# Optimization experiments

Measured on AMD Instinct MI355X. Metric: run time of the kernel, lower is better.

## Reference

```python
import jax, jax.numpy as jnp
import numpy as np
from functools import partial

LEAK = 1.0 / 3.0   # scn default leakiness 0.333
EPS = 1e-4         # scn BatchNormalization default eps


def linkey(c, S):
    return (c[..., 0] * S + c[..., 1]) * S + c[..., 2]


def sub_offsets(K):
    r = K // 2
    g = np.stack(np.meshgrid(*([np.arange(-r, r + 1)] * 3), indexing='ij'), -1).reshape(-1, 3)
    return jnp.asarray(g, jnp.int32)


def down_offsets(s):
    g = np.stack(np.meshgrid(*([np.arange(s)] * 3), indexing='ij'), -1).reshape(-1, 3)
    return jnp.asarray(g, jnp.int32)


@partial(jax.checkpoint, static_argnums=(4, 5))
def sparse_conv(out_coords, in_coords, in_feats, W, S_in, stride, offsets):
    """Rulebook gather-GEMM-scatter via sorted-key binary search.
    out_coords [M,3], in_coords [N,3] sorted by linearized key, in_feats [N,Cin],
    W [K3,Cin,Cout]. Submanifold: stride=1, centered offsets, out_coords==in_coords.
    Strided scn.Convolution: offsets 0..stride-1, out sites = unique(in//stride)."""
    in_keys = linkey(in_coords, S_in)  # sorted [N]
    Nin = in_keys.shape[0]

    def body(acc, kw):
        off, Wk = kw
        child = out_coords * stride + off                       # [M,3]
        valid = jnp.all((child >= 0) & (child < S_in), axis=-1)
        nkey = linkey(child, S_in)
        idx = jnp.searchsorted(in_keys, nkey)
        idxc = jnp.clip(idx, 0, Nin - 1)
        found = valid & (in_keys[idxc] == nkey)
        g = jnp.where(found[:, None], in_feats[idxc], 0.0)      # gather, zero for inactive
        return acc + g @ Wk, None

    acc0 = jnp.zeros((out_coords.shape[0], W.shape[-1]), in_feats.dtype)
    acc, _ = jax.lax.scan(body, acc0, (offsets, W))
    return acc


def bn_lrelu(x, g, b):
    m = x.mean(0)
    v = x.var(0)
    y = (x - m) * (g / jnp.sqrt(v + EPS)) + b
    return jnp.where(y > 0, y, LEAK * y)


def lrelu(x):
    return jnp.where(x > 0, x, LEAK * x)


def forward_core(floats, c0, c1, c2, c3, c4):
    (feats0, W_init, Wd1, gd1, bd1, W11a, g11, b11, W11b,
     W12a, g12, b12, W12b, Wd2, gd2, bd2,
     W21a, g21, b21, W21b, W22a, g22, b22, W22b,
     Wd3, gd3, bd3, Wd4, gd4, bd4, W2, b2, W3, b3) = floats
    o3 = sub_offsets(3)
    x = sparse_conv(c0, c0, feats0, W_init, 512, 1, sub_offsets(7))                 # [N0,64] @512
    x = bn_lrelu(sparse_conv(c1, c0, x, Wd1, 512, 2, down_offsets(2)), gd1, bd1)    # [N1,64] @256
    res = x
    h = bn_lrelu(sparse_conv(c1, c1, x, W11a, 256, 1, o3), g11, b11)
    x = lrelu(sparse_conv(c1, c1, h, W11b, 256, 1, o3) + res)
    res = x
    h = bn_lrelu(sparse_conv(c1, c1, x, W12a, 256, 1, o3), g12, b12)
    x = lrelu(sparse_conv(c1, c1, h, W12b, 256, 1, o3) + res)
    x = bn_lrelu(sparse_conv(c2, c1, x, Wd2, 256, 2, down_offsets(2)), gd2, bd2)    # [N2,128] @128
    res = x
    h = bn_lrelu(sparse_conv(c2, c2, x, W21a, 128, 1, o3), g21, b21)
    x = lrelu(sparse_conv(c2, c2, h, W21b, 128, 1, o3) + res)
    res = x
    h = bn_lrelu(sparse_conv(c2, c2, x, W22a, 128, 1, o3), g22, b22)
    x = lrelu(sparse_conv(c2, c2, h, W22b, 128, 1, o3) + res)
    x = bn_lrelu(sparse_conv(c3, c2, x, Wd3, 128, 4, down_offsets(4)), gd3, bd3)    # [N3,64] @32
    x = bn_lrelu(sparse_conv(c4, c3, x, Wd4, 32, 4, down_offsets(4)), gd4, bd4)     # [N4,2]  @8
    # SparseToDense -> dense [2,8,8,8], then torch .view(-1, 2*8*8*8) (channel-major)
    k4 = linkey(c4, 8)
    dense = jnp.zeros((8 * 8 * 8, 2), x.dtype).at[k4].set(x)    # [512,2]
    flat = dense.T.reshape(1, -1)                               # [1,1024]
    v = jax.nn.elu(flat @ W2 + b2)
    return jax.nn.sigmoid(v @ W3 + b3)                          # [1,1]


def _decode(k, S):
    a = k // (S * S)
    r = k % (S * S)
    return np.stack([a, r // S, r % S], -1).astype(np.int32)


def setup_inputs() -> dict:
    rng = np.random.default_rng(0)
    N0 = 50000
    k0 = np.unique(rng.integers(0, 512 ** 3, size=N0 + 20000))[:N0]
    c0 = _decode(k0, 512)
    c1 = _decode(np.unique((c0[:, 0].astype(np.int64) // 2 * 256 + c0[:, 1] // 2) * 256 + c0[:, 2] // 2), 256)
    c2 = _decode(np.unique((c1[:, 0].astype(np.int64) // 2 * 128 + c1[:, 1] // 2) * 128 + c1[:, 2] // 2), 128)
    c3 = _decode(np.unique((c2[:, 0].astype(np.int64) // 4 * 32 + c2[:, 1] // 4) * 32 + c2[:, 2] // 4), 32)
    c4 = _decode(np.unique((c3[:, 0].astype(np.int64) // 4 * 8 + c3[:, 1] // 4) * 8 + c3[:, 2] // 4), 8)
    key = jax.random.key(0)
    ks = jax.random.split(key, 20)

    def w(i, shape, fan):
        return jax.random.normal(ks[i], shape, jnp.float32) / np.float32(np.sqrt(fan))

    return dict(
        feats0=jax.random.normal(ks[0], (N0, 1), jnp.float32),
        W_init=w(1, (343, 1, 64), 343.0),
        Wd1=w(2, (8, 64, 64), 8 * 64), gd1=jnp.ones(64), bd1=jnp.zeros(64),
        W11a=w(3, (27, 64, 64), 27 * 64), g11=jnp.ones(64), b11=jnp.zeros(64),
        W11b=w(4, (27, 64, 64), 27 * 64),
        W12a=w(5, (27, 64, 64), 27 * 64), g12=jnp.ones(64), b12=jnp.zeros(64),
        W12b=w(6, (27, 64, 64), 27 * 64),
        Wd2=w(7, (8, 64, 128), 8 * 64), gd2=jnp.ones(128), bd2=jnp.zeros(128),
        W21a=w(8, (27, 128, 128), 27 * 128), g21=jnp.ones(128), b21=jnp.zeros(128),
        W21b=w(9, (27, 128, 128), 27 * 128),
        W22a=w(10, (27, 128, 128), 27 * 128), g22=jnp.ones(128), b22=jnp.zeros(128),
        W22b=w(11, (27, 128, 128), 27 * 128),
        Wd3=w(12, (64, 128, 64), 64 * 128), gd3=jnp.ones(64), bd3=jnp.zeros(64),
        Wd4=w(13, (64, 64, 2), 64 * 64), gd4=jnp.ones(2), bd4=jnp.zeros(2),
        W2=w(14, (1024, 2), 1024.0), b2=jnp.zeros(2),
        W3=w(15, (2, 1), 2.0), b3=jnp.zeros(1),
        coords0=jnp.asarray(c0), coords1=jnp.asarray(c1), coords2=jnp.asarray(c2),
        coords3=jnp.asarray(c3), coords4=jnp.asarray(c4),
    )


def reference(feats0, W_init, Wd1, gd1, bd1, W11a, g11, b11, W11b, W12a, g12, b12, W12b,
              Wd2, gd2, bd2, W21a, g21, b21, W21b, W22a, g22, b22, W22b,
              Wd3, gd3, bd3, Wd4, gd4, bd4, W2, b2, W3, b3,
              coords0, coords1, coords2, coords3, coords4):
    floats = (feats0, W_init, Wd1, gd1, bd1, W11a, g11, b11, W11b, W12a, g12, b12, W12b,
              Wd2, gd2, bd2, W21a, g21, b21, W21b, W22a, g22, b22, W22b,
              Wd3, gd3, bd3, Wd4, gd4, bd4, W2, b2, W3, b3)
    return forward_core(floats, coords0, coords1, coords2, coords3, coords4)
```

## Files before the change

### kernel.cpp

```cpp
#include <hip/hip_runtime.h>

#define LEAKF (1.0f/3.0f)
#define BN_EPS 1e-4f

__device__ __forceinline__ unsigned hmix(int key) {
    unsigned h = (unsigned)key * 2654435761u;
    h ^= h >> 15;
    return h;
}

__device__ __forceinline__ int hlookup(const int* __restrict__ hk,
                                       const int* __restrict__ hv,
                                       int mask, int key) {
    unsigned h = hmix(key) & (unsigned)mask;
    while (true) {
        int k = hk[h];
        if (k == key) return hv[h];
        if (k == -1) return -1;
        h = (h + 1) & (unsigned)mask;
    }
}

__device__ __forceinline__ float bnl(float v, float s, float h) {
    v = v * s + h;
    return v > 0.f ? v : v * LEAKF;
}

__global__ __launch_bounds__(256) void build_hash_bm_all(
    int B0, int B1, int B2,
    int N0, const int* __restrict__ c0, int* __restrict__ hk0, int* __restrict__ hv0,
    int m0, unsigned* __restrict__ bm0,
    int N1, const int* __restrict__ c1, int* __restrict__ hk1, int* __restrict__ hv1,
    int m1, unsigned* __restrict__ bm1,
    int N2, const int* __restrict__ c2, int* __restrict__ hk2, int* __restrict__ hv2,
    int m2, unsigned* __restrict__ bm2,
    int N3, const int* __restrict__ c3, int* __restrict__ hk3, int* __restrict__ hv3,
    int m3) {
    const int* coords; int* hk; int* hv; unsigned* bm; int mask, S, N, i;
    int b = blockIdx.x;
    if (b < B0)           { coords = c0; hk = hk0; hv = hv0; bm = bm0; mask = m0; S = 512; N = N0; i = b * 256 + threadIdx.x; }
    else if (b < B0 + B1) { coords = c1; hk = hk1; hv = hv1; bm = bm1; mask = m1; S = 256; N = N1; i = (b - B0) * 256 + threadIdx.x; }
    else if (b < B0 + B1 + B2) { coords = c2; hk = hk2; hv = hv2; bm = bm2; mask = m2; S = 128; N = N2; i = (b - B0 - B1) * 256 + threadIdx.x; }
    else                  { coords = c3; hk = hk3; hv = hv3; bm = nullptr; mask = m3; S = 32; N = N3; i = (b - B0 - B1 - B2) * 256 + threadIdx.x; }
    if (i >= N) return;
    int key = (coords[3 * i] * S + coords[3 * i + 1]) * S + coords[3 * i + 2];
    if (bm) atomicOr(&bm[key >> 5], 1u << (key & 31));
    unsigned h = hmix(key) & (unsigned)mask;
    while (true) {
        int old = atomicCAS(&hk[h], -1, key);
        if (old == -1 || old == key) { hv[h] = i; break; }
        h = (h + 1) & (unsigned)mask;
    }
}

__global__ __launch_bounds__(256) void rb_sub_bm(
    int B1,
    int N1, const int* __restrict__ c1, const unsigned* __restrict__ bm1,
    const int* __restrict__ hk1, const int* __restrict__ hv1, int m1,
    int2* __restrict__ rb1, int* __restrict__ cnt1, int cap1,
    int N2, const int* __restrict__ c2, const unsigned* __restrict__ bm2,
    const int* __restrict__ hk2, const int* __restrict__ hv2, int m2,
    int2* __restrict__ rb2, int* __restrict__ cnt2, int cap2) {
    __shared__ int lcnt[27];
    __shared__ int lbase[27];
    int tid = threadIdx.x;
    if (tid < 27) lcnt[tid] = 0;
    __syncthreads();
    const int* coords; const unsigned* bm; const int* hk; const int* hv;
    int mask, S, N, t; int2* pairs; int* counts; int cap;
    if (blockIdx.x < B1) {
        coords = c1; bm = bm1; hk = hk1; hv = hv1; mask = m1; S = 256; N = N1;
        pairs = rb1; counts = cnt1; cap = cap1; t = blockIdx.x * 256 + tid;
    } else {
        coords = c2; bm = bm2; hk = hk2; hv = hv2; mask = m2; S = 128; N = N2;
        pairs = rb2; counts = cnt2; cap = cap2; t = (blockIdx.x - B1) * 256 + tid;
    }
    unsigned bits = 0;
    int m = 0, kmin = 0, z = 0, dx = 0, dy = 0;
    int rk[3], ix[3];
    if (t < N * 9) {
        m = t / 9;
        int od = t - m * 9;
        dx = od / 3 - 1;
        dy = od - (od / 3) * 3 - 1;
        int x = coords[3 * m] + dx;
        int y = coords[3 * m + 1] + dy;
        z = coords[3 * m + 2];
        if ((unsigned)x < (unsigned)S && (unsigned)y < (unsigned)S) {
            int zmin = z - 1 < 0 ? 0 : z - 1;
            int zmax = z + 1 > S - 1 ? S - 1 : z + 1;
            kmin = (x * S + y) * S + zmin;
            int wi = kmin >> 5, sh = kmin & 31, nb = zmax - zmin + 1;
            unsigned long long w =
                ((unsigned long long)bm[wi + 1] << 32) | (unsigned long long)bm[wi];
            bits = (unsigned)((w >> sh) & ((1u << nb) - 1u));
            if (dx == 0 && dy == 0) bits &= ~(1u << (z - zmin));
            unsigned tmp = bits;
            int nf = 0;
            while (tmp) {
                int bb = __ffs(tmp) - 1;
                tmp &= tmp - 1;
                ix[nf] = hlookup(hk, hv, mask, kmin + bb);
                int dz = (kmin & (S - 1)) + bb - z;
                int k = (dx + 1) * 9 + (dy + 1) * 3 + (dz + 1);
                rk[nf] = atomicAdd(&lcnt[k], 1);
                nf++;
            }
        }
    }
    __syncthreads();
    if (tid < 27 && lcnt[tid] > 0) lbase[tid] = atomicAdd(&counts[tid], lcnt[tid]);
    __syncthreads();
    {
        unsigned tmp = bits;
        int j = 0;
        while (tmp) {
            int bb = __ffs(tmp) - 1;
            tmp &= tmp - 1;
            int dz = (kmin & (S - 1)) + bb - z;
            int k = (dx + 1) * 9 + (dy + 1) * 3 + (dz + 1);
            int p = lbase[k] + rk[j];
            if (p < cap) pairs[(size_t)k * cap + p] = make_int2(m, ix[j]);
            j++;
        }
    }
}

__global__ __launch_bounds__(256) void rb_down_all(
    int B1, int B2,
    int N0, const int* __restrict__ c0, const int* __restrict__ hk1,
    const int* __restrict__ hv1, int m1, int2* __restrict__ rbD1,
    int* __restrict__ cntD1, int capD1,
    int N1, const int* __restrict__ c1, const int* __restrict__ hk2,
    const int* __restrict__ hv2, int m2, int2* __restrict__ rbD2,
    int* __restrict__ cntD2, int capD2,
    int N2, const int* __restrict__ c2, const int* __restrict__ hk3,
    const int* __restrict__ hv3, int m3, int2* __restrict__ rbD3,
    int* __restrict__ cntD3, int capD3) {
    __shared__ int lcnt[64];
    __shared__ int lbase[64];
    int tid = threadIdx.x;
    const int* cin; const int* hk; const int* hv;
    int mask, Sout, s, Nin, i; int2* pairs; int* counts; int cap;
    int b = blockIdx.x;
    if (b < B1) {
        cin = c0; hk = hk1; hv = hv1; mask = m1; Sout = 256; s = 2; Nin = N0;
        pairs = rbD1; counts = cntD1; cap = capD1; i = b * 256 + tid;
    } else if (b < B1 + B2) {
        cin = c1; hk = hk2; hv = hv2; mask = m2; Sout = 128; s = 2; Nin = N1;
        pairs = rbD2; counts = cntD2; cap = capD2; i = (b - B1) * 256 + tid;
    } else {
        cin = c2; hk = hk3; hv = hv3; mask = m3; Sout = 32; s = 4; Nin = N2;
        pairs = rbD3; counts = cntD3; cap = capD3; i = (b - B1 - B2) * 256 + tid;
    }
    int K3 = s * s * s;
    if (tid < K3) lcnt[tid] = 0;
    __syncthreads();
    int k = -1, m = -1, rank = 0;
    if (i < Nin) {
        int x = cin[3 * i], y = cin[3 * i + 1], z = cin[3 * i + 2];
        k = ((x % s) * s + (y % s)) * s + (z % s);
        int key = ((x / s) * Sout + (y / s)) * Sout + (z / s);
        m = hlookup(hk, hv, mask, key);
        rank = atomicAdd(&lcnt[k], 1);
    }
    __syncthreads();
    if (tid < K3 && lcnt[tid] > 0) lbase[tid] = atomicAdd(&counts[tid], lcnt[tid]);
    __syncthreads();
    if (i < Nin) {
        int p = lbase[k] + rank;
        if (p < cap) pairs[(size_t)k * cap + p] = make_int2(m, i);
    }
}

__global__ __launch_bounds__(256) void init_probe(
    int total, int chunk, const int* __restrict__ c0, const unsigned* __restrict__ bm,
    const int* __restrict__ hk, const int* __restrict__ hv, int mask,
    int2* __restrict__ pairs, int* __restrict__ pcount, int cap) {
    __shared__ int lcnt, lbase;
    int tid = threadIdx.x;
    if (tid == 0) lcnt = 0;
    __syncthreads();
    int b = blockIdx.x;
    int nb = (b & 7) * chunk + (b >> 3);
    int t = nb * 256 + tid;
    unsigned bits = 0;
    int m = -1, kmin = 0, z = 0, dx = 0, dy = 0, rank = 0;
    if (t < total) {
        m = t / 49;
        int od = t - m * 49;
        dx = od / 7 - 3;
        dy = od - (od / 7) * 7 - 3;
        int x = c0[3 * m] + dx;
        int y = c0[3 * m + 1] + dy;
        z = c0[3 * m + 2];
        if ((unsigned)x < 512u && (unsigned)y < 512u) {
            int zmin = z - 3 < 0 ? 0 : z - 3;
            int zmax = z + 3 > 511 ? 511 : z + 3;
            kmin = (x * 512 + y) * 512 + zmin;
            int wi = kmin >> 5, sh = kmin & 31, nb2 = zmax - zmin + 1;
            unsigned long long w =
                ((unsigned long long)bm[wi + 1] << 32) | (unsigned long long)bm[wi];
            bits = (unsigned)((w >> sh) & ((1u << nb2) - 1u));
            if (dx == 0 && dy == 0) bits &= ~(1u << (z - zmin));
            if (bits) rank = atomicAdd(&lcnt, __popc(bits));
        }
    }
    __syncthreads();
    if (tid == 0 && lcnt > 0) lbase = atomicAdd(pcount, lcnt);
    __syncthreads();
    while (bits) {
        int b2 = __ffs(bits) - 1;
        bits &= bits - 1;
        int nkey = kmin + b2;
        int idx = hlookup(hk, hv, mask, nkey);
        int dz = (kmin & 511) + b2 - z;
        int k = (dx + 3) * 49 + (dy + 3) * 7 + (dz + 3);
        int p = lbase + rank++;
        if (p < cap) pairs[p] = make_int2(m, idx | (k << 17));
    }
}

__global__ __launch_bounds__(256) void init_center(
    int N0, const float* __restrict__ f0, const float* __restrict__ W,
    float* __restrict__ out) {
    int t = blockIdx.x * 256 + threadIdx.x;
    if (t >= N0 * 64) return;
    int m = t >> 6, co = t & 63;
    out[t] = f0[m] * W[171 * 64 + co];
}

__global__ __launch_bounds__(256) void init_apply(
    const int2* __restrict__ pairs, const int* __restrict__ pcount, int cap,
    const float* __restrict__ f0, const float* __restrict__ W,
    float* __restrict__ out) {
    int P = min(*pcount, cap);
    int t = blockIdx.x * 256 + threadIdx.x;
    if (t >= P * 64) return;
    int p = t >> 6, co = t & 63;
    int2 pr = pairs[p];
    int idx = pr.y & 0x1FFFF, k = pr.y >> 17;
    atomicAdd(&out[(size_t)pr.x * 64 + co], f0[idx] * W[k * 64 + co]);
}

template <int C, int TS, bool BNF>
__global__ __launch_bounds__(256) void center_gemm(
    int N, const float* __restrict__ inF, const float* __restrict__ Wc,
    float* __restrict__ out, const float* __restrict__ scp,
    const float* __restrict__ shp) {
    constexpr int C4 = C / 4;
    constexpr int SP = TS / 8;
    __shared__ float sW[C * 64];
    __shared__ float4 sRow[TS * C4];
    int tid = threadIdx.x;
    int t0 = blockIdx.x * TS;
    int co0 = blockIdx.y << 6;
    for (int e = tid; e < C * 16; e += 256) {
        int ci = e >> 4, c4 = e & 15;
        ((float4*)sW)[e] = *(const float4*)(Wc + (size_t)ci * C + co0 + c4 * 4);
    }
    for (int e = tid; e < TS * C4; e += 256) {
        int p = e / C4, c4 = e - p * C4;
        float4 v = make_float4(0.f, 0.f, 0.f, 0.f);
        if (t0 + p < N) {
            v = ((const float4*)inF)[(size_t)(t0 + p) * C4 + c4];
            if (BNF) {
                float4 s4 = ((const float4*)scp)[c4];
                float4 h4 = ((const float4*)shp)[c4];
                v.x = bnl(v.x, s4.x, h4.x);
                v.y = bnl(v.y, s4.y, h4.y);
                v.z = bnl(v.z, s4.z, h4.z);
                v.w = bnl(v.w, s4.w, h4.w);
            }
        }
        sRow[e] = v;
    }
    __syncthreads();
    int co = tid & 31, sg = tid >> 5;
    float accA[SP], accB[SP];
#pragma unroll
    for (int j = 0; j < SP; j++) { accA[j] = 0.f; accB[j] = 0.f; }
    for (int c4 = 0; c4 < C4; c4++) {
        float a0 = sW[(c4 * 4 + 0) * 64 + co];
        float a1 = sW[(c4 * 4 + 1) * 64 + co];
        float a2 = sW[(c4 * 4 + 2) * 64 + co];
        float a3 = sW[(c4 * 4 + 3) * 64 + co];
        float b0 = sW[(c4 * 4 + 0) * 64 + co + 32];
        float b1 = sW[(c4 * 4 + 1) * 64 + co + 32];
        float b2 = sW[(c4 * 4 + 2) * 64 + co + 32];
        float b3 = sW[(c4 * 4 + 3) * 64 + co + 32];
#pragma unroll
        for (int j = 0; j < SP; j++) {
            float4 r = sRow[(sg * SP + j) * C4 + c4];
            accA[j] += r.x * a0 + r.y * a1 + r.z * a2 + r.w * a3;
            accB[j] += r.x * b0 + r.y * b1 + r.z * b2 + r.w * b3;
        }
    }
#pragma unroll
    for (int j = 0; j < SP; j++) {
        int p = sg * SP + j;
        if (t0 + p < N) {
            out[(size_t)(t0 + p) * C + co0 + co] = accA[j];
            out[(size_t)(t0 + p) * C + co0 + co + 32] = accB[j];
        }
    }
}

template <int CIN, int P, int MODE>
__global__ __launch_bounds__(256) void pair_gemm(
    const float* __restrict__ inF, const float* __restrict__ inF2,
    const float* __restrict__ W, float* __restrict__ out,
    const int2* __restrict__ pairs, const int* __restrict__ counts,
    int cap, int chunksPerK, int totalNb, int COUT,
    const float* __restrict__ scp, const float* __restrict__ shp) {
    constexpr int C4 = CIN / 4;
    constexpr int SP = P / 8;
    __shared__ float sW[CIN * 64];
    __shared__ float4 sRow[P * C4];
    __shared__ int sM[P];
    __shared__ int sIdx[P];
    int b = blockIdx.x;
    int nb = (b & 7) * (gridDim.x >> 3) + (b >> 3);
    if (nb >= totalNb) return;
    int k = nb / chunksPerK;
    int chunk = nb - k * chunksPerK;
    int cnt = min(counts[k], cap);
    int base = chunk * P;
    if (base >= cnt) return;
    int Pact = min(P, cnt - base);
    int tid = threadIdx.x;
    if (tid < P) {
        if (tid < Pact) {
            int2 pr = pairs[(size_t)k * cap + base + tid];
            sM[tid] = pr.x;
            sIdx[tid] = pr.y;
        } else {
            sM[tid] = -1;
            sIdx[tid] = 0;
        }
    }
    __syncthreads();
    int co0 = blockIdx.y << 6;
    const float* gW = W + (size_t)k * CIN * COUT + co0;
    for (int e = tid; e < CIN * 16; e += 256) {
        int ci = e >> 4, c4 = e & 15;
        ((float4*)sW)[e] = *(const float4*)(gW + (size_t)ci * COUT + c4 * 4);
    }
    for (int e = tid; e < P * C4; e += 256) {
        int p = e / C4, c4 = e - p * C4;
        float4 v = make_float4(0.f, 0.f, 0.f, 0.f);
        if (p < Pact) {
            v = ((const float4*)inF)[(size_t)sIdx[p] * C4 + c4];
            if (MODE == 1) {
                float4 s4 = ((const float4*)scp)[c4];
                float4 h4 = ((const float4*)shp)[c4];
                v.x = bnl(v.x, s4.x, h4.x);
                v.y = bnl(v.y, s4.y, h4.y);
                v.z = bnl(v.z, s4.z, h4.z);
                v.w = bnl(v.w, s4.w, h4.w);
            } else if (MODE == 2) {
                float4 u = ((const float4*)inF2)[(size_t)sIdx[p] * C4 + c4];
                v.x += u.x; v.y += u.y; v.z += u.z; v.w += u.w;
                v.x = v.x > 0.f ? v.x : v.x * LEAKF;
                v.y = v.y > 0.f ? v.y : v.y * LEAKF;
                v.z = v.z > 0.f ? v.z : v.z * LEAKF;
                v.w = v.w > 0.f ? v.w : v.w * LEAKF;
            }
        }
        sRow[e] = v;
    }
    __syncthreads();
    int co = tid & 31, sg = tid >> 5;
    float accA[SP], accB[SP];
#pragma unroll
    for (int j = 0; j < SP; j++) { accA[j] = 0.f; accB[j] = 0.f; }
    for (int c4 = 0; c4 < C4; c4++) {
        float a0 = sW[(c4 * 4 + 0) * 64 + co];
        float a1 = sW[(c4 * 4 + 1) * 64 + co];
        float a2 = sW[(c4 * 4 + 2) * 64 + co];
        float a3 = sW[(c4 * 4 + 3) * 64 + co];
        float b0 = sW[(c4 * 4 + 0) * 64 + co + 32];
        float b1 = sW[(c4 * 4 + 1) * 64 + co + 32];
        float b2 = sW[(c4 * 4 + 2) * 64 + co + 32];
        float b3 = sW[(c4 * 4 + 3) * 64 + co + 32];
#pragma unroll
        for (int j = 0; j < SP; j++) {
            float4 r = sRow[(sg * SP + j) * C4 + c4];
            accA[j] += r.x * a0 + r.y * a1 + r.z * a2 + r.w * a3;
            accB[j] += r.x * b0 + r.y * b1 + r.z * b2 + r.w * b3;
        }
    }
#pragma unroll
    for (int j = 0; j < SP; j++) {
        int p = sg * SP + j;
        if (p < Pact) {
            atomicAdd(&out[(size_t)sM[p] * COUT + co0 + co], accA[j]);
            atomicAdd(&out[(size_t)sM[p] * COUT + co0 + co + 32], accB[j]);
        }
    }
}

__global__ __launch_bounds__(64) void convd4_kernel(
    int M, const int* __restrict__ oc, const float* __restrict__ x3,
    const float* __restrict__ W, float* __restrict__ out4,
    const int* __restrict__ hk, const int* __restrict__ hv, int mask,
    const float* __restrict__ scp, const float* __restrict__ shp) {
    __shared__ int sIdx[64];
    __shared__ int sK[64];
    __shared__ int sCount;
    int m = blockIdx.x, tid = threadIdx.x;
    int cx = oc[3 * m], cy = oc[3 * m + 1], cz = oc[3 * m + 2];
    if (tid == 0) sCount = 0;
    __syncthreads();
    {
        int k = tid;
        int a = k >> 4, b = (k >> 2) & 3, c = k & 3;
        int x = cx * 4 + a, y = cy * 4 + b, z = cz * 4 + c;
        int key = (x * 32 + y) * 32 + z;
        int idx = hlookup(hk, hv, mask, key);
        if (idx >= 0) { int p = atomicAdd(&sCount, 1); sIdx[p] = idx; sK[p] = k; }
    }
    __syncthreads();
    int cnt = sCount;
    float s = scp[tid], h = shp[tid];
    float a0 = 0.f, a1 = 0.f;
    for (int j = 0; j < cnt; j++) {
        int idx = sIdx[j], k = sK[j];
        float f = bnl(x3[(size_t)idx * 64 + tid], s, h);
        const float* wk = W + ((size_t)k * 64 + tid) * 2;
        a0 += f * wk[0];
        a1 += f * wk[1];
    }
    for (int o = 32; o > 0; o >>= 1) {
        a0 += __shfl_down(a0, o);
        a1 += __shfl_down(a1, o);
    }
    if (tid == 0) { out4[2 * m] = a0; out4[2 * m + 1] = a1; }
}

__global__ __launch_bounds__(256) void bn_reduce_fin(
    const float4* __restrict__ X4, int total4, int B4, int C, int Cmask, float invN,
    const float* __restrict__ g, const float* __restrict__ b,
    float* __restrict__ sums, int* __restrict__ done,
    float* __restrict__ sc, float* __restrict__ sh) {
    __shared__ float sS[128];
    __shared__ float sQ[128];
    __shared__ int isLast;
    int tid = threadIdx.x;
    if (tid < C) { sS[tid] = 0.f; sQ[tid] = 0.f; }
    __syncthreads();
    int base4 = blockIdx.x * B4;
    int end4 = min(base4 + B4, total4);
    float s0 = 0.f, s1 = 0.f, s2 = 0.f, s3 = 0.f;
    float q0 = 0.f, q1 = 0.f, q2 = 0.f, q3 = 0.f;
    for (int e4 = base4 + tid; e4 < end4; e4 += 256) {
        float4 v = X4[e4];
        s0 += v.x; q0 += v.x * v.x;
        s1 += v.y; q1 += v.y * v.y;
        s2 += v.z; q2 += v.z * v.z;
        s3 += v.w; q3 += v.w * v.w;
    }
    int c0 = (4 * (base4 + tid)) & Cmask;
    atomicAdd(&sS[c0], s0);               atomicAdd(&sQ[c0], q0);
    atomicAdd(&sS[(c0 + 1) & Cmask], s1); atomicAdd(&sQ[(c0 + 1) & Cmask], q1);
    atomicAdd(&sS[(c0 + 2) & Cmask], s2); atomicAdd(&sQ[(c0 + 2) & Cmask], q2);
    atomicAdd(&sS[(c0 + 3) & Cmask], s3); atomicAdd(&sQ[(c0 + 3) & Cmask], q3);
    __syncthreads();
    if (tid < C) {
        atomicAdd(&sums[tid], sS[tid]);
        atomicAdd(&sums[128 + tid], sQ[tid]);
    }
    __syncthreads();
    if (tid == 0) {
        __threadfence();
        int t = atomicAdd(done, 1);
        isLast = (t == (int)gridDim.x - 1);
    }
    __syncthreads();
    if (isLast) {
        if (tid < C) {
            float v1 = atomicAdd(&sums[tid], 0.0f);
            float v2 = atomicAdd(&sums[128 + tid], 0.0f);
            float mean = v1 * invN;
            float var = v2 * invN - mean * mean;
            float s = g[tid] / sqrtf(var + BN_EPS);
            sc[tid] = s;
            sh[tid] = b[tid] - mean * s;
            sums[tid] = 0.f;
            sums[128 + tid] = 0.f;
        }
        if (tid == 0) *done = 0;
    }
}

__global__ __launch_bounds__(256) void add_lrelu_bn(const float4* __restrict__ A,
                                                    const float4* __restrict__ X,
                                                    float4* __restrict__ Y, int total4,
                                                    int C4mask,
                                                    const float* __restrict__ scp,
                                                    const float* __restrict__ shp) {
    int e = blockIdx.x * 256 + threadIdx.x;
    if (e >= total4) return;
    int c4 = e & C4mask;
    float4 s4 = ((const float4*)scp)[c4];
    float4 h4 = ((const float4*)shp)[c4];
    float4 a = A[e], x = X[e], v;
    v.x = a.x + bnl(x.x, s4.x, h4.x);
    v.y = a.y + bnl(x.y, s4.y, h4.y);
    v.z = a.z + bnl(x.z, s4.z, h4.z);
    v.w = a.w + bnl(x.w, s4.w, h4.w);
    v.x = v.x > 0.f ? v.x : v.x * LEAKF;
    v.y = v.y > 0.f ? v.y : v.y * LEAKF;
    v.z = v.z > 0.f ? v.z : v.z * LEAKF;
    v.w = v.w > 0.f ? v.w : v.w * LEAKF;
    Y[e] = v;
}

__global__ __launch_bounds__(256) void bn_scatter(int M, const int* __restrict__ c4,
                                                  const float* __restrict__ x4,
                                                  const float* __restrict__ sc,
                                                  const float* __restrict__ sh,
                                                  float* __restrict__ dense) {
    int i = blockIdx.x * 256 + threadIdx.x;
    if (i >= 2 * M) return;
    int m = i >> 1, co = i & 1;
    float v = x4[i] * sc[co] + sh[co];
    v = v > 0.f ? v : v * LEAKF;
    int key = (c4[3 * m] * 8 + c4[3 * m + 1]) * 8 + c4[3 * m + 2];
    dense[key * 2 + co] = v;
}

__global__ __launch_bounds__(256) void head_kernel(const float* __restrict__ dense,
                                                   const float* __restrict__ W2,
                                                   const float* __restrict__ b2,
                                                   const float* __restrict__ W3,
                                                   const float* __restrict__ b3,
                                                   float* __restrict__ out) {
    __shared__ float r0[256];
    __shared__ float r1[256];
    int tid = threadIdx.x;
    float a0 = 0.f, a1 = 0.f;
    for (int j = tid; j < 1024; j += 256) {
        int co = j >> 9, k = j & 511;
        float f = dense[k * 2 + co];
        a0 += f * W2[2 * j];
        a1 += f * W2[2 * j + 1];
    }
    r0[tid] = a0;
    r1[tid] = a1;
    __syncthreads();
    for (int s = 128; s > 0; s >>= 1) {
        if (tid < s) { r0[tid] += r0[tid + s]; r1[tid] += r1[tid + s]; }
        __syncthreads();
    }
    if (tid == 0) {
        float v0 = r0[0] + b2[0];
        float v1 = r1[0] + b2[1];
        v0 = v0 > 0.f ? v0 : expm1f(v0);
        v1 = v1 > 0.f ? v1 : expm1f(v1);
        float z = v0 * W3[0] + v1 * W3[1] + b3[0];
        out[0] = 1.f / (1.f + expf(-z));
    }
}

extern "C" void kernel_launch(void* const* d_in, const int* in_sizes, int n_in,
                              void* d_out, int out_size, void* d_ws, size_t ws_size,
                              hipStream_t stream) {
    const float* F0    = (const float*)d_in[0];
    const float* Winit = (const float*)d_in[1];
    const float* Wd1   = (const float*)d_in[2];
    const float* gd1   = (const float*)d_in[3];
    const float* bd1   = (const float*)d_in[4];
    const float* W11a  = (const float*)d_in[5];
    const float* g11   = (const float*)d_in[6];
    const float* b11   = (const float*)d_in[7];
    const float* W11b  = (const float*)d_in[8];
    const float* W12a  = (const float*)d_in[9];
    const float* g12   = (const float*)d_in[10];
    const float* b12   = (const float*)d_in[11];
    const float* W12b  = (const float*)d_in[12];
    const float* Wd2   = (const float*)d_in[13];
    const float* gd2   = (const float*)d_in[14];
    const float* bd2   = (const float*)d_in[15];
    const float* W21a  = (const float*)d_in[16];
    const float* g21   = (const float*)d_in[17];
    const float* b21   = (const float*)d_in[18];
    const float* W21b  = (const float*)d_in[19];
    const float* W22a  = (const float*)d_in[20];
    const float* g22   = (const float*)d_in[21];
    const float* b22   = (const float*)d_in[22];
    const float* W22b  = (const float*)d_in[23];
    const float* Wd3   = (const float*)d_in[24];
    const float* gd3   = (const float*)d_in[25];
    const float* bd3   = (const float*)d_in[26];
    const float* Wd4   = (const float*)d_in[27];
    const float* gd4   = (const float*)d_in[28];
    const float* bd4   = (const float*)d_in[29];
    const float* W2    = (const float*)d_in[30];
    const float* b2    = (const float*)d_in[31];
    const float* W3    = (const float*)d_in[32];
    const float* b3    = (const float*)d_in[33];
    const int* c0 = (const int*)d_in[34];
    const int* c1 = (const int*)d_in[35];
    const int* c2 = (const int*)d_in[36];
    const int* c3 = (const int*)d_in[37];
    const int* c4 = (const int*)d_in[38];
    int N0 = in_sizes[34] / 3, N1 = in_sizes[35] / 3, N2 = in_sizes[36] / 3;
    int N3 = in_sizes[37] / 3, N4 = in_sizes[38] / 3;

    char* base = (char*)d_ws;
    size_t off = 0;
    auto alloc = [&](size_t bytes) -> void* {
        void* p = base + off;
        off = (off + bytes + 255) & ~(size_t)255;
        return p;
    };
    const int CAP0 = 262144, CAP = 131072, CAP3 = 65536;
    size_t hs_off = off;
    int* hk0 = (int*)alloc((size_t)CAP0 * 4);
    int* hv0 = (int*)alloc((size_t)CAP0 * 4);
    int* hk1 = (int*)alloc((size_t)CAP * 4);
    int* hv1 = (int*)alloc((size_t)CAP * 4);
    int* hk2 = (int*)alloc((size_t)CAP * 4);
    int* hv2 = (int*)alloc((size_t)CAP * 4);
    int* hk3 = (int*)alloc((size_t)CAP3 * 4);
    int* hv3 = (int*)alloc((size_t)CAP3 * 4);
    size_t he_off = off;
    size_t zs_off = off;
    float* sums = (float*)alloc(256 * 4);
    float* scb = (float*)alloc(8 * 128 * 4);
    float* shb = (float*)alloc(8 * 128 * 4);
    float* dense = (float*)alloc(1024 * 4);
    float* x4 = (float*)alloc(1032 * 4);
    int* counts = (int*)alloc(136 * 4);
    unsigned* bm1 = (unsigned*)alloc((size_t)(524288 + 2) * 4);
    unsigned* bm2 = (unsigned*)alloc((size_t)(65536 + 2) * 4);
    size_t ze_off = off;
    int* cntS1 = counts, *cntS2 = counts + 27, *cntD1 = counts + 54, *cntD2 = counts + 62,
       * cntD3 = counts + 70;
    int* done = counts + 134;
    int* pcount = counts + 135;
    const int CAP_S1 = 1024, CAP_S2 = 4096, CAP_D1 = 8192, CAP_D2 = 8192, CAP_D3 = 1024;
    const int CAPP = 16384;
    int2* pairs0 = (int2*)alloc((size_t)CAPP * 8);
    int2* rbS1 = (int2*)alloc((size_t)27 * CAP_S1 * 8);
    int2* rbS2 = (int2*)alloc((size_t)27 * CAP_S2 * 8);
    int2* rbD1 = (int2*)alloc((size_t)8 * CAP_D1 * 8);
    int2* rbD2 = (int2*)alloc((size_t)8 * CAP_D2 * 8);
    int2* rbD3 = (int2*)alloc((size_t)64 * CAP_D3 * 8);
    size_t relems = (size_t)N0 * 64;
    if ((size_t)N2 * 128 > relems) relems = (size_t)N2 * 128;
    float* R1 = (float*)alloc(relems * 4);
    float* R2 = (float*)alloc(relems * 4);
    float* R3 = (float*)alloc(relems * 4);
    unsigned* bm0 = (unsigned*)R1;

    hipMemsetAsync(base + hs_off, 0xFF, he_off - hs_off, stream);
    hipMemsetAsync(base + zs_off, 0x00, ze_off - zs_off, stream);
    hipMemsetAsync(bm0, 0x00, (size_t)(1 << 24) + 64, stream);

    int Bh0 = (N0 + 255) / 256, Bh1 = (N1 + 255) / 256, Bh2 = (N2 + 255) / 256,
        Bh3 = (N3 + 255) / 256;
    build_hash_bm_all<<<Bh0 + Bh1 + Bh2 + Bh3, 256, 0, stream>>>(
        Bh0, Bh1, Bh2,
        N0, c0, hk0, hv0, CAP0 - 1, bm0,
        N1, c1, hk1, hv1, CAP - 1, bm1,
        N2, c2, hk2, hv2, CAP - 1, bm2,
        N3, c3, hk3, hv3, CAP3 - 1);
    int Bs1 = (N1 * 9 + 255) / 256, Bs2 = (N2 * 9 + 255) / 256;
    rb_sub_bm<<<Bs1 + Bs2, 256, 0, stream>>>(
        Bs1,
        N1, c1, bm1, hk1, hv1, CAP - 1, rbS1, cntS1, CAP_S1,
        N2, c2, bm2, hk2, hv2, CAP - 1, rbS2, cntS2, CAP_S2);
    rb_down_all<<<Bh0 + Bh1 + Bh2, 256, 0, stream>>>(
        Bh0, Bh1,
        N0, c0, hk1, hv1, CAP - 1, rbD1, cntD1, CAP_D1,
        N1, c1, hk2, hv2, CAP - 1, rbD2, cntD2, CAP_D2,
        N2, c2, hk3, hv3, CAP3 - 1, rbD3, cntD3, CAP_D3);

    auto bnstats = [&](const float* X, int N, int C, const float* g, const float* b,
                       int slot) {
        int total4 = (N * C + 3) >> 2;
        int B4 = 32 * C;
        int grid = (total4 + B4 - 1) / B4;
        bn_reduce_fin<<<grid, 256, 0, stream>>>((const float4*)X, total4, B4, C, C - 1,
                                                1.0f / (float)N, g, b, sums, done,
                                                scb + slot * 128, shb + slot * 128);
    };
    const int CH_S1 = CAP_S1 / 64;
    const int CH_S2 = CAP_S2 / 32;
    const int CH_D12 = CAP_D1 / 64;
    const int CH_D3 = CAP_D3 / 32;
    auto sub64 = [&](const float* X, const float* W, float* Y, int slot) {
        if (slot >= 0) {
            center_gemm<64, 64, true><<<dim3((N1 + 63) / 64, 1), 256, 0, stream>>>(
                N1, X, W + 13 * 64 * 64, Y, scb + slot * 128, shb + slot * 128);
            pair_gemm<64, 64, 1><<<dim3(27 * CH_S1, 1), 256, 0, stream>>>(
                X, nullptr, W, Y, rbS1, cntS1, CAP_S1, CH_S1, 27 * CH_S1, 64,
                scb + slot * 128, shb + slot * 128);
        } else {
            center_gemm<64, 64, false><<<dim3((N1 + 63) / 64, 1), 256, 0, stream>>>(
                N1, X, W + 13 * 64 * 64, Y, nullptr, nullptr);
            pair_gemm<64, 64, 0><<<dim3(27 * CH_S1, 1), 256, 0, stream>>>(
                X, nullptr, W, Y, rbS1, cntS1, CAP_S1, CH_S1, 27 * CH_S1, 64,
                nullptr, nullptr);
        }
    };
    auto sub128 = [&](const float* X, const float* W, float* Y, int slot) {
        if (slot >= 0) {
            center_gemm<128, 48, true><<<dim3((N2 + 47) / 48, 2), 256, 0, stream>>>(
                N2, X, W + 13 * 128 * 128, Y, scb + slot * 128, shb + slot * 128);
            pair_gemm<128, 32, 1><<<dim3(27 * CH_S2, 2), 256, 0, stream>>>(
                X, nullptr, W, Y, rbS2, cntS2, CAP_S2, CH_S2, 27 * CH_S2, 128,
                scb + slot * 128, shb + slot * 128);
        } else {
            center_gemm<128, 48, false><<<dim3((N2 + 47) / 48, 2), 256, 0, stream>>>(
                N2, X, W + 13 * 128 * 128, Y, nullptr, nullptr);
            pair_gemm<128, 32, 0><<<dim3(27 * CH_S2, 2), 256, 0, stream>>>(
                X, nullptr, W, Y, rbS2, cntS2, CAP_S2, CH_S2, 27 * CH_S2, 128,
                nullptr, nullptr);
        }
    };

    int totProbe = N0 * 49;
    int Gp = (totProbe + 255) / 256;
    int chunkP = (Gp + 7) / 8;
    init_probe<<<8 * chunkP, 256, 0, stream>>>(totProbe, chunkP, c0, bm0,
                                               hk0, hv0, CAP0 - 1, pairs0, pcount, CAPP);
    init_center<<<(N0 * 64 + 255) / 256, 256, 0, stream>>>(N0, F0, Winit, R3);
    init_apply<<<(CAPP * 64) / 256, 256, 0, stream>>>(pairs0, pcount, CAPP, F0, Winit, R3);

    hipMemsetAsync(R1, 0, (size_t)N1 * 64 * 4, stream);
    pair_gemm<64, 64, 0><<<dim3(8 * CH_D12, 1), 256, 0, stream>>>(
        R3, nullptr, Wd1, R1, rbD1, cntD1, CAP_D1, CH_D12, 8 * CH_D12, 64,
        nullptr, nullptr);
    bnstats(R1, N1, 64, gd1, bd1, 0);

    sub64(R1, W11a, R2, 0);
    bnstats(R2, N1, 64, g11, b11, 1);
    sub64(R2, W11b, R3, 1);
    add_lrelu_bn<<<(N1 * 16 + 255) / 256, 256, 0, stream>>>(
        (const float4*)R3, (const float4*)R1, (float4*)R2, N1 * 16, 15, scb, shb);
    sub64(R2, W12a, R3, -1);
    bnstats(R3, N1, 64, g12, b12, 2);
    sub64(R3, W12b, R1, 2);

    hipMemsetAsync(R3, 0, (size_t)N2 * 128 * 4, stream);
    pair_gemm<64, 64, 2><<<dim3(8 * CH_D12, 2), 256, 0, stream>>>(
        R1, R2, Wd2, R3, rbD2, cntD2, CAP_D2, CH_D12, 8 * CH_D12, 128,
        nullptr, nullptr);
    bnstats(R3, N2, 128, gd2, bd2, 3);

    sub128(R3, W21a, R1, 3);
    bnstats(R1, N2, 128, g21, b21, 4);
    sub128(R1, W21b, R2, 4);
    add_lrelu_bn<<<(N2 * 32 + 255) / 256, 256, 0, stream>>>(
        (const float4*)R2, (const float4*)R3, (float4*)R1, N2 * 32, 31,
        scb + 3 * 128, shb + 3 * 128);
    sub128(R1, W22a, R2, -1);
    bnstats(R2, N2, 128, g22, b22, 5);
    sub128(R2, W22b, R3, 5);

    hipMemsetAsync(R2, 0, (size_t)N3 * 64 * 4, stream);
    pair_gemm<128, 32, 2><<<dim3(64 * CH_D3, 1), 256, 0, stream>>>(
        R3, R1, Wd3, R2, rbD3, cntD3, CAP_D3, CH_D3, 64 * CH_D3, 64,
        nullptr, nullptr);
    bnstats(R2, N3, 64, gd3, bd3, 6);

    convd4_kernel<<<N4, 64, 0, stream>>>(N4, c4, R2, Wd4, x4, hk3, hv3, CAP3 - 1,
                                         scb + 6 * 128, shb + 6 * 128);
    bnstats(x4, N4, 2, gd4, bd4, 7);
    bn_scatter<<<(2 * N4 + 255) / 256, 256, 0, stream>>>(N4, c4, x4, scb + 7 * 128,
                                                         shb + 7 * 128, dense);

    head_kernel<<<1, 256, 0, stream>>>(dense, W2, b2, W3, b3, (float*)d_out);
}
```

Before: 1.101 ms.

## Fuse tail kernels, loop output slabs in pair_gemm, batch init probe over y

The 7x7x7 init probe now gives each thread one dx and all seven dy rows, so N0*7 threads replace N0*49 and there is a single shared atomic per thread. pair_gemm loops over 64-wide output-channel slabs inside one block instead of using a second grid dimension, so the gathered input rows are loaded once and reused across slabs. The final conv, the BN statistics, the scatter and the head are fused into one kernel whose last block, picked by an atomic ticket, runs the reduction and head. The aim is fewer launches and less redundant gathering, at the cost of fewer parallel blocks in pair_gemm and serial work in a single 64-thread tail block.

```diff
diff --git a/kernel.cpp b/kernel.cpp
--- a/kernel.cpp
+++ b/kernel.cpp
@@ -184,40 +184,58 @@
     int b = blockIdx.x;
     int nb = (b & 7) * chunk + (b >> 3);
     int t = nb * 256 + tid;
-    unsigned bits = 0;
-    int m = -1, kmin = 0, z = 0, dx = 0, dy = 0, rank = 0;
+    unsigned bitsArr[7];
+    int kminArr[7];
+#pragma unroll
+    for (int j = 0; j < 7; j++) { bitsArr[j] = 0; kminArr[j] = 0; }
+    int m = -1, z = 0, dx = 0, rank = 0, found = 0;
     if (t < total) {
-        m = t / 49;
-        int od = t - m * 49;
-        dx = od / 7 - 3;
-        dy = od - (od / 7) * 7 - 3;
+        m = t / 7;
+        dx = t - m * 7 - 3;
         int x = c0[3 * m] + dx;
-        int y = c0[3 * m + 1] + dy;
+        int cy = c0[3 * m + 1];
         z = c0[3 * m + 2];
-        if ((unsigned)x < 512u && (unsigned)y < 512u) {
+        if ((unsigned)x < 512u) {
             int zmin = z - 3 < 0 ? 0 : z - 3;
             int zmax = z + 3 > 511 ? 511 : z + 3;
-            kmin = (x * 512 + y) * 512 + zmin;
-            int wi = kmin >> 5, sh = kmin & 31, nb2 = zmax - zmin + 1;
-            unsigned long long w =
-                ((unsigned long long)bm[wi + 1] << 32) | (unsigned long long)bm[wi];
-            bits = (unsigned)((w >> sh) & ((1u << nb2) - 1u));
-            if (dx == 0 && dy == 0) bits &= ~(1u << (z - zmin));
-            if (bits) rank = atomicAdd(&lcnt, __popc(bits));
-        }
-    }
+            int nbits = zmax - zmin + 1;
+#pragma unroll
+            for (int j = 0; j < 7; j++) {
+                int y = cy + j - 3;
+                if ((unsigned)y < 512u) {
+                    int kmin = (x * 512 + y) * 512 + zmin;
+                    kminArr[j] = kmin;
+                    int wi = kmin >> 5, sh = kmin & 31;
+                    unsigned long long w =
+                        ((unsigned long long)bm[wi + 1] << 32) | (unsigned long long)bm[wi];
+                    unsigned bits = (unsigned)((w >> sh) & ((1u << nbits) - 1u));
+                    if (dx == 0 && j == 3) bits &= ~(1u << (z - zmin));
+                    bitsArr[j] = bits;
+                    found += __popc(bits);
+                }
+            }
+        }
+    }
+    if (found) rank = atomicAdd(&lcnt, found);
     __syncthreads();
     if (tid == 0 && lcnt > 0) lbase = atomicAdd(pcount, lcnt);
     __syncthreads();
-    while (bits) {
-        int b2 = __ffs(bits) - 1;
-        bits &= bits - 1;
-        int nkey = kmin + b2;
-        int idx = hlookup(hk, hv, mask, nkey);
-        int dz = (kmin & 511) + b2 - z;
-        int k = (dx + 3) * 49 + (dy + 3) * 7 + (dz + 3);
-        int p = lbase + rank++;
-        if (p < cap) pairs[p] = make_int2(m, idx | (k << 17));
+    if (found) {
+        int p = lbase + rank;
+#pragma unroll
+        for (int j = 0; j < 7; j++) {
+            unsigned bits = bitsArr[j];
+            while (bits) {
+                int b2 = __ffs(bits) - 1;
+                bits &= bits - 1;
+                int nkey = kminArr[j] + b2;
+                int idx = hlookup(hk, hv, mask, nkey);
+                int dz = (kminArr[j] & 511) + b2 - z;
+                int k = (dx + 3) * 49 + j * 7 + (dz + 3);
+                if (p < cap) pairs[p] = make_int2(m, idx | (k << 17));
+                p++;
+            }
+        }
     }
 }
 
@@ -311,7 +329,7 @@
     const float* __restrict__ inF, const float* __restrict__ inF2,
     const float* __restrict__ W, float* __restrict__ out,
     const int2* __restrict__ pairs, const int* __restrict__ counts,
-    int cap, int chunksPerK, int totalNb, int COUT,
+    int cap, int chunksPerK, int totalNb, int COUT, int nslab,
     const float* __restrict__ scp, const float* __restrict__ shp) {
     constexpr int C4 = CIN / 4;
     constexpr int SP = P / 8;
@@ -340,102 +358,69 @@
         }
     }
     __syncthreads();
-    int co0 = blockIdx.y << 6;
-    const float* gW = W + (size_t)k * CIN * COUT + co0;
-    for (int e = tid; e < CIN * 16; e += 256) {
-        int ci = e >> 4, c4 = e & 15;
-        ((float4*)sW)[e] = *(const float4*)(gW + (size_t)ci * COUT + c4 * 4);
-    }
-    for (int e = tid; e < P * C4; e += 256) {
-        int p = e / C4, c4 = e - p * C4;
-        float4 v = make_float4(0.f, 0.f, 0.f, 0.f);
-        if (p < Pact) {
-            v = ((const float4*)inF)[(size_t)sIdx[p] * C4 + c4];
-            if (MODE == 1) {
-                float4 s4 = ((const float4*)scp)[c4];
-                float4 h4 = ((const float4*)shp)[c4];
-                v.x = bnl(v.x, s4.x, h4.x);
-                v.y = bnl(v.y, s4.y, h4.y);
-                v.z = bnl(v.z, s4.z, h4.z);
-                v.w = bnl(v.w, s4.w, h4.w);
-            } else if (MODE == 2) {
-                float4 u = ((const float4*)inF2)[(size_t)sIdx[p] * C4 + c4];
-                v.x += u.x; v.y += u.y; v.z += u.z; v.w += u.w;
-                v.x = v.x > 0.f ? v.x : v.x * LEAKF;
-                v.y = v.y > 0.f ? v.y : v.y * LEAKF;
-                v.z = v.z > 0.f ? v.z : v.z * LEAKF;
-                v.w = v.w > 0.f ? v.w : v.w * LEAKF;
+    int co = tid & 31, sg = tid >> 5;
+    for (int s = 0; s < nslab; s++) {
+        int co0 = s << 6;
+        if (s > 0) __syncthreads();
+        const float* gW = W + (size_t)k * CIN * COUT + co0;
+        for (int e = tid; e < CIN * 16; e += 256) {
+            int ci = e >> 4, c4 = e & 15;
+            ((float4*)sW)[e] = *(const float4*)(gW + (size_t)ci * COUT + c4 * 4);
+        }
+        if (s == 0) {
+            for (int e = tid; e < P * C4; e += 256) {
+                int p = e / C4, c4 = e - p * C4;
+                float4 v = make_float4(0.f, 0.f, 0.f, 0.f);
+                if (p < Pact) {
+                    v = ((const float4*)inF)[(size_t)sIdx[p] * C4 + c4];
+                    if (MODE == 1) {
+                        float4 s4 = ((const float4*)scp)[c4];
+                        float4 h4 = ((const float4*)shp)[c4];
+                        v.x = bnl(v.x, s4.x, h4.x);
+                        v.y = bnl(v.y, s4.y, h4.y);
+                        v.z = bnl(v.z, s4.z, h4.z);
+                        v.w = bnl(v.w, s4.w, h4.w);
+                    } else if (MODE == 2) {
+                        float4 u = ((const float4*)inF2)[(size_t)sIdx[p] * C4 + c4];
+                        v.x += u.x; v.y += u.y; v.z += u.z; v.w += u.w;
+                        v.x = v.x > 0.f ? v.x : v.x * LEAKF;
+                        v.y = v.y > 0.f ? v.y : v.y * LEAKF;
+                        v.z = v.z > 0.f ? v.z : v.z * LEAKF;
+                        v.w = v.w > 0.f ? v.w : v.w * LEAKF;
+                    }
+                }
+                sRow[e] = v;
             }
         }
-        sRow[e] = v;
-    }
-    __syncthreads();
-    int co = tid & 31, sg = tid >> 5;
-    float accA[SP], accB[SP];
+        __syncthreads();
+        float accA[SP], accB[SP];
 #pragma unroll
-    for (int j = 0; j < SP; j++) { accA[j] = 0.f; accB[j] = 0.f; }
-    for (int c4 = 0; c4 < C4; c4++) {
-        float a0 = sW[(c4 * 4 + 0) * 64 + co];
-        float a1 = sW[(c4 * 4 + 1) * 64 + co];
-        float a2 = sW[(c4 * 4 + 2) * 64 + co];
-        float a3 = sW[(c4 * 4 + 3) * 64 + co];
-        float b0 = sW[(c4 * 4 + 0) * 64 + co + 32];
-        float b1 = sW[(c4 * 4 + 1) * 64 + co + 32];
-        float b2 = sW[(c4 * 4 + 2) * 64 + co + 32];
-        float b3 = sW[(c4 * 4 + 3) * 64 + co + 32];
+        for (int j = 0; j < SP; j++) { accA[j] = 0.f; accB[j] = 0.f; }
+        for (int c4 = 0; c4 < C4; c4++) {
+            float a0 = sW[(c4 * 4 + 0) * 64 + co];
+            float a1 = sW[(c4 * 4 + 1) * 64 + co];
+            float a2 = sW[(c4 * 4 + 2) * 64 + co];
+            float a3 = sW[(c4 * 4 + 3) * 64 + co];
+            float b0 = sW[(c4 * 4 + 0) * 64 + co + 32];
+            float b1 = sW[(c4 * 4 + 1) * 64 + co + 32];
+            float b2 = sW[(c4 * 4 + 2) * 64 + co + 32];
+            float b3 = sW[(c4 * 4 + 3) * 64 + co + 32];
+#pragma unroll
+            for (int j = 0; j < SP; j++) {
+                float4 r = sRow[(sg * SP + j) * C4 + c4];
+                accA[j] += r.x * a0 + r.y * a1 + r.z * a2 + r.w * a3;
+                accB[j] += r.x * b0 + r.y * b1 + r.z * b2 + r.w * b3;
+            }
+        }
 #pragma unroll
         for (int j = 0; j < SP; j++) {
-            float4 r = sRow[(sg * SP + j) * C4 + c4];
-            accA[j] += r.x * a0 + r.y * a1 + r.z * a2 + r.w * a3;
-            accB[j] += r.x * b0 + r.y * b1 + r.z * b2 + r.w * b3;
-        }
-    }
-#pragma unroll
-    for (int j = 0; j < SP; j++) {
-        int p = sg * SP + j;
-        if (p < Pact) {
-            atomicAdd(&out[(size_t)sM[p] * COUT + co0 + co], accA[j]);
-            atomicAdd(&out[(size_t)sM[p] * COUT + co0 + co + 32], accB[j]);
-        }
-    }
-}
-
-__global__ __launch_bounds__(64) void convd4_kernel(
-    int M, const int* __restrict__ oc, const float* __restrict__ x3,
-    const float* __restrict__ W, float* __restrict__ out4,
-    const int* __restrict__ hk, const int* __restrict__ hv, int mask,
-    const float* __restrict__ scp, const float* __restrict__ shp) {
-    __shared__ int sIdx[64];
-    __shared__ int sK[64];
-    __shared__ int sCount;
-    int m = blockIdx.x, tid = threadIdx.x;
-    int cx = oc[3 * m], cy = oc[3 * m + 1], cz = oc[3 * m + 2];
-    if (tid == 0) sCount = 0;
-    __syncthreads();
-    {
-        int k = tid;
-        int a = k >> 4, b = (k >> 2) & 3, c = k & 3;
-        int x = cx * 4 + a, y = cy * 4 + b, z = cz * 4 + c;
-        int key = (x * 32 + y) * 32 + z;
-        int idx = hlookup(hk, hv, mask, key);
-        if (idx >= 0) { int p = atomicAdd(&sCount, 1); sIdx[p] = idx; sK[p] = k; }
-    }
-    __syncthreads();
-    int cnt = sCount;
-    float s = scp[tid], h = shp[tid];
-    float a0 = 0.f, a1 = 0.f;
-    for (int j = 0; j < cnt; j++) {
-        int idx = sIdx[j], k = sK[j];
-        float f = bnl(x3[(size_t)idx * 64 + tid], s, h);
-        const float* wk = W + ((size_t)k * 64 + tid) * 2;
-        a0 += f * wk[0];
-        a1 += f * wk[1];
-    }
-    for (int o = 32; o > 0; o >>= 1) {
-        a0 += __shfl_down(a0, o);
-        a1 += __shfl_down(a1, o);
-    }
-    if (tid == 0) { out4[2 * m] = a0; out4[2 * m + 1] = a1; }
+            int p = sg * SP + j;
+            if (p < Pact) {
+                atomicAdd(&out[(size_t)sM[p] * COUT + co0 + co], accA[j]);
+                atomicAdd(&out[(size_t)sM[p] * COUT + co0 + co + 32], accB[j]);
+            }
+        }
+    }
 }
 
 __global__ __launch_bounds__(256) void bn_reduce_fin(
@@ -516,46 +501,97 @@
     Y[e] = v;
 }
 
-__global__ __launch_bounds__(256) void bn_scatter(int M, const int* __restrict__ c4,
-                                                  const float* __restrict__ x4,
-                                                  const float* __restrict__ sc,
-                                                  const float* __restrict__ sh,
-                                                  float* __restrict__ dense) {
-    int i = blockIdx.x * 256 + threadIdx.x;
-    if (i >= 2 * M) return;
-    int m = i >> 1, co = i & 1;
-    float v = x4[i] * sc[co] + sh[co];
-    v = v > 0.f ? v : v * LEAKF;
-    int key = (c4[3 * m] * 8 + c4[3 * m + 1]) * 8 + c4[3 * m + 2];
-    dense[key * 2 + co] = v;
-}
-
-__global__ __launch_bounds__(256) void head_kernel(const float* __restrict__ dense,
-                                                   const float* __restrict__ W2,
-                                                   const float* __restrict__ b2,
-                                                   const float* __restrict__ W3,
-                                                   const float* __restrict__ b3,
-                                                   float* __restrict__ out) {
-    __shared__ float r0[256];
-    __shared__ float r1[256];
-    int tid = threadIdx.x;
+__global__ __launch_bounds__(64) void tail_kernel(
+    int M, const int* __restrict__ oc, const float* __restrict__ x3,
+    const float* __restrict__ W, float* __restrict__ x4,
+    const int* __restrict__ hk, const int* __restrict__ hv, int mask,
+    const float* __restrict__ scp, const float* __restrict__ shp,
+    const float* __restrict__ g4, const float* __restrict__ b4,
+    const float* __restrict__ W2, const float* __restrict__ b2,
+    const float* __restrict__ W3, const float* __restrict__ b3,
+    int* __restrict__ ticket, float* __restrict__ out) {
+    __shared__ int sIdx[64];
+    __shared__ int sK[64];
+    __shared__ int sCount;
+    __shared__ int isLast;
+    __shared__ float sDense[1024];
+    __shared__ float sS[2], sQ[2], ssc[2], ssh[2];
+    int m = blockIdx.x, tid = threadIdx.x;
+    int cx = oc[3 * m], cy = oc[3 * m + 1], cz = oc[3 * m + 2];
+    if (tid == 0) sCount = 0;
+    __syncthreads();
+    {
+        int k = tid;
+        int a = k >> 4, b = (k >> 2) & 3, c = k & 3;
+        int x = cx * 4 + a, y = cy * 4 + b, z = cz * 4 + c;
+        int key = (x * 32 + y) * 32 + z;
+        int idx = hlookup(hk, hv, mask, key);
+        if (idx >= 0) { int p = atomicAdd(&sCount, 1); sIdx[p] = idx; sK[p] = k; }
+    }
+    __syncthreads();
+    int cnt = sCount;
+    float s = scp[tid], h = shp[tid];
     float a0 = 0.f, a1 = 0.f;
-    for (int j = tid; j < 1024; j += 256) {
+    for (int j = 0; j < cnt; j++) {
+        int idx = sIdx[j], k = sK[j];
+        float f = bnl(x3[(size_t)idx * 64 + tid], s, h);
+        const float* wk = W + ((size_t)k * 64 + tid) * 2;
+        a0 += f * wk[0];
+        a1 += f * wk[1];
+    }
+    for (int o = 32; o > 0; o >>= 1) {
+        a0 += __shfl_down(a0, o);
+        a1 += __shfl_down(a1, o);
+    }
+    if (tid == 0) { x4[2 * m] = a0; x4[2 * m + 1] = a1; }
+    __threadfence();
+    if (tid == 0) {
+        int t = atomicAdd(ticket, 1);
+        isLast = (t == (int)gridDim.x - 1);
+    }
+    __syncthreads();
+    if (!isLast) return;
+    if (tid < 2) { sS[tid] = 0.f; sQ[tid] = 0.f; }
+    for (int i = tid; i < 1024; i += 64) sDense[i] = 0.f;
+    __syncthreads();
+    float ls = 0.f, lq = 0.f;
+    for (int i = tid; i < 2 * M; i += 64) {
+        float v = atomicAdd(&x4[i], 0.0f);
+        ls += v; lq += v * v;
+    }
+    atomicAdd(&sS[tid & 1], ls);
+    atomicAdd(&sQ[tid & 1], lq);
+    __syncthreads();
+    if (tid < 2) {
+        float mean = sS[tid] / (float)M;
+        float var = sQ[tid] / (float)M - mean * mean;
+        float sc = g4[tid] / sqrtf(var + BN_EPS);
+        ssc[tid] = sc;
+        ssh[tid] = b4[tid] - mean * sc;
+    }
+    __syncthreads();
+    for (int i = tid; i < 2 * M; i += 64) {
+        int mm = i >> 1, co = i & 1;
+        float v = atomicAdd(&x4[i], 0.0f) * ssc[co] + ssh[co];
+        v = v > 0.f ? v : v * LEAKF;
+        int key = (oc[3 * mm] * 8 + oc[3 * mm + 1]) * 8 + oc[3 * mm + 2];
+        sDense[key * 2 + co] = v;
+    }
+    __syncthreads();
+    float h0 = 0.f, h1 = 0.f;
+    for (int j = tid; j < 1024; j += 64) {
         int co = j >> 9, k = j & 511;
-        float f = dense[k * 2 + co];
-        a0 += f * W2[2 * j];
-        a1 += f * W2[2 * j + 1];
-    }
-    r0[tid] = a0;
-    r1[tid] = a1;
-    __syncthreads();
-    for (int s = 128; s > 0; s >>= 1) {
-        if (tid < s) { r0[tid] += r0[tid + s]; r1[tid] += r1[tid + s]; }
-        __syncthreads();
+        float f = sDense[k * 2 + co];
+        h0 += f * W2[2 * j];
+        h1 += f * W2[2 * j + 1];
+    }
+    for (int o = 32; o > 0; o >>= 1) {
+        h0 += __shfl_down(h0, o);
+        h1 += __shfl_down(h1, o);
     }
     if (tid == 0) {
-        float v0 = r0[0] + b2[0];
-        float v1 = r1[0] + b2[1];
+        float v0 = h0 + b2[0];
+        float v1 = h1 + b2[1];
         v0 = v0 > 0.f ? v0 : expm1f(v0);
         v1 = v1 > 0.f ? v1 : expm1f(v1);
         float z = v0 * W3[0] + v1 * W3[1] + b3[0];
@@ -630,7 +666,6 @@
     float* sums = (float*)alloc(256 * 4);
     float* scb = (float*)alloc(8 * 128 * 4);
     float* shb = (float*)alloc(8 * 128 * 4);
-    float* dense = (float*)alloc(1024 * 4);
     float* x4 = (float*)alloc(1032 * 4);
     int* counts = (int*)alloc(136 * 4);
     unsigned* bm1 = (unsigned*)alloc((size_t)(524288 + 2) * 4);
@@ -695,14 +730,14 @@
         if (slot >= 0) {
             center_gemm<64, 64, true><<<dim3((N1 + 63) / 64, 1), 256, 0, stream>>>(
                 N1, X, W + 13 * 64 * 64, Y, scb + slot * 128, shb + slot * 128);
-            pair_gemm<64, 64, 1><<<dim3(27 * CH_S1, 1), 256, 0, stream>>>(
-                X, nullptr, W, Y, rbS1, cntS1, CAP_S1, CH_S1, 27 * CH_S1, 64,
+            pair_gemm<64, 64, 1><<<27 * CH_S1, 256, 0, stream>>>(
+                X, nullptr, W, Y, rbS1, cntS1, CAP_S1, CH_S1, 27 * CH_S1, 64, 1,
                 scb + slot * 128, shb + slot * 128);
         } else {
             center_gemm<64, 64, false><<<dim3((N1 + 63) / 64, 1), 256, 0, stream>>>(
                 N1, X, W + 13 * 64 * 64, Y, nullptr, nullptr);
-            pair_gemm<64, 64, 0><<<dim3(27 * CH_S1, 1), 256, 0, stream>>>(
-                X, nullptr, W, Y, rbS1, cntS1, CAP_S1, CH_S1, 27 * CH_S1, 64,
+            pair_gemm<64, 64, 0><<<27 * CH_S1, 256, 0, stream>>>(
+                X, nullptr, W, Y, rbS1, cntS1, CAP_S1, CH_S1, 27 * CH_S1, 64, 1,
                 nullptr, nullptr);
         }
     };
@@ -710,19 +745,19 @@
         if (slot >= 0) {
             center_gemm<128, 48, true><<<dim3((N2 + 47) / 48, 2), 256, 0, stream>>>(
                 N2, X, W + 13 * 128 * 128, Y, scb + slot * 128, shb + slot * 128);
-            pair_gemm<128, 32, 1><<<dim3(27 * CH_S2, 2), 256, 0, stream>>>(
-                X, nullptr, W, Y, rbS2, cntS2, CAP_S2, CH_S2, 27 * CH_S2, 128,
+            pair_gemm<128, 32, 1><<<27 * CH_S2, 256, 0, stream>>>(
+                X, nullptr, W, Y, rbS2, cntS2, CAP_S2, CH_S2, 27 * CH_S2, 128, 2,
                 scb + slot * 128, shb + slot * 128);
         } else {
             center_gemm<128, 48, false><<<dim3((N2 + 47) / 48, 2), 256, 0, stream>>>(
                 N2, X, W + 13 * 128 * 128, Y, nullptr, nullptr);
-            pair_gemm<128, 32, 0><<<dim3(27 * CH_S2, 2), 256, 0, stream>>>(
-                X, nullptr, W, Y, rbS2, cntS2, CAP_S2, CH_S2, 27 * CH_S2, 128,
+            pair_gemm<128, 32, 0><<<27 * CH_S2, 256, 0, stream>>>(
+                X, nullptr, W, Y, rbS2, cntS2, CAP_S2, CH_S2, 27 * CH_S2, 128, 2,
                 nullptr, nullptr);
         }
     };
 
-    int totProbe = N0 * 49;
+    int totProbe = N0 * 7;
     int Gp = (totProbe + 255) / 256;
     int chunkP = (Gp + 7) / 8;
     init_probe<<<8 * chunkP, 256, 0, stream>>>(totProbe, chunkP, c0, bm0,
@@ -731,8 +766,8 @@
     init_apply<<<(CAPP * 64) / 256, 256, 0, stream>>>(pairs0, pcount, CAPP, F0, Winit, R3);
 
     hipMemsetAsync(R1, 0, (size_t)N1 * 64 * 4, stream);
-    pair_gemm<64, 64, 0><<<dim3(8 * CH_D12, 1), 256, 0, stream>>>(
-        R3, nullptr, Wd1, R1, rbD1, cntD1, CAP_D1, CH_D12, 8 * CH_D12, 64,
+    pair_gemm<64, 64, 0><<<8 * CH_D12, 256, 0, stream>>>(
+        R3, nullptr, Wd1, R1, rbD1, cntD1, CAP_D1, CH_D12, 8 * CH_D12, 64, 1,
         nullptr, nullptr);
     bnstats(R1, N1, 64, gd1, bd1, 0);
 
@@ -746,8 +781,8 @@
     sub64(R3, W12b, R1, 2);
 
     hipMemsetAsync(R3, 0, (size_t)N2 * 128 * 4, stream);
-    pair_gemm<64, 64, 2><<<dim3(8 * CH_D12, 2), 256, 0, stream>>>(
-        R1, R2, Wd2, R3, rbD2, cntD2, CAP_D2, CH_D12, 8 * CH_D12, 128,
+    pair_gemm<64, 64, 2><<<8 * CH_D12, 256, 0, stream>>>(
+        R1, R2, Wd2, R3, rbD2, cntD2, CAP_D2, CH_D12, 8 * CH_D12, 128, 2,
         nullptr, nullptr);
     bnstats(R3, N2, 128, gd2, bd2, 3);
 
@@ -762,16 +797,12 @@
     sub128(R2, W22b, R3, 5);
 
     hipMemsetAsync(R2, 0, (size_t)N3 * 64 * 4, stream);
-    pair_gemm<128, 32, 2><<<dim3(64 * CH_D3, 1), 256, 0, stream>>>(
-        R3, R1, Wd3, R2, rbD3, cntD3, CAP_D3, CH_D3, 64 * CH_D3, 64,
+    pair_gemm<128, 32, 2><<<64 * CH_D3, 256, 0, stream>>>(
+        R3, R1, Wd3, R2, rbD3, cntD3, CAP_D3, CH_D3, 64 * CH_D3, 64, 1,
         nullptr, nullptr);
     bnstats(R2, N3, 64, gd3, bd3, 6);
 
-    convd4_kernel<<<N4, 64, 0, stream>>>(N4, c4, R2, Wd4, x4, hk3, hv3, CAP3 - 1,
-                                         scb + 6 * 128, shb + 6 * 128);
-    bnstats(x4, N4, 2, gd4, bd4, 7);
-    bn_scatter<<<(2 * N4 + 255) / 256, 256, 0, stream>>>(N4, c4, x4, scb + 7 * 128,
-                                                         shb + 7 * 128, dense);
-
-    head_kernel<<<1, 256, 0, stream>>>(dense, W2, b2, W3, b3, (float*)d_out);
-}
+    tail_kernel<<<N4, 64, 0, stream>>>(N4, c4, R2, Wd4, x4, hk3, hv3, CAP3 - 1,
+                                       scb + 6 * 128, shb + 6 * 128, gd4, bd4,
+                                       W2, b2, W3, b3, done, (float*)d_out);
+}
```

After: 1.095 ms, median of 3. Within noise of the previous version (-0.5%).
